# Optimization experiments

Measured on AMD Instinct MI355X. Metric: run time of the kernel, lower is better.

Reference implementation:

```python
import jax, jax.numpy as jnp
import numpy as np

N = 50000      # nodes
E = 800000     # edges (avg degree 16)
F_IN = 128     # num_features
HID = 128      # hidden_channels
C = 4          # num_labeled_classes


def setup_inputs() -> dict:
    key = jax.random.key(0)
    ks = jax.random.split(key, 12)
    x = jax.random.normal(ks[0], (N, F_IN), dtype=jnp.float32)
    edge_index = jax.random.randint(ks[1], (2, E), 0, N, dtype=jnp.int32)

    def lin(k, fan_in, fan_out):
        return (jax.random.normal(k, (fan_in, fan_out), dtype=jnp.float32)
                / np.float32(np.sqrt(fan_in)))

    return {
        "x": x,
        "edge_index": edge_index,
        # layer 0: SAGEConv(F_IN, HID) -> lin_l (with bias) on aggregated neighbors, lin_r on self
        "Wl0": lin(ks[2], F_IN, HID), "bl0": jnp.zeros((HID,), jnp.float32), "Wr0": lin(ks[3], F_IN, HID),
        # layer 1: SAGEConv(HID, HID)
        "Wl1": lin(ks[4], HID, HID), "bl1": jnp.zeros((HID,), jnp.float32), "Wr1": lin(ks[5], HID, HID),
        # layer 2: SAGEConv(HID, C)
        "Wl2": lin(ks[6], HID, C), "bl2": jnp.zeros((C,), jnp.float32), "Wr2": lin(ks[7], HID, C),
    }


def _sage_conv(x, src, dst, inv_deg, Wl, bl, Wr):
    # gather neighbor features [E, d], mean-aggregate at destination nodes
    msg = x[src]
    agg = jax.ops.segment_sum(msg, dst, num_segments=N)  # [N, d]
    mean = agg * inv_deg[:, None]
    # out = lin_l(mean_j) + lin_r(x_i)   (PyG SAGEConv default, mean aggr)
    return mean @ Wl + bl + x @ Wr


def reference(x, edge_index, Wl0, bl0, Wr0, Wl1, bl1, Wr1, Wl2, bl2, Wr2):
    src = edge_index[0]
    dst = edge_index[1]
    # in-degree of each destination node, clamped to 1 (isolated nodes -> 0 mean)
    deg = jax.ops.segment_sum(jnp.ones((E,), x.dtype), dst, num_segments=N)
    inv_deg = jnp.where(deg > 0, 1.0 / jnp.maximum(deg, 1.0), 0.0)

    h = _sage_conv(x, src, dst, inv_deg, Wl0, bl0, Wr0)
    h = jax.nn.relu(h)
    # dropout(p=0.5) is identity in eval mode
    h2 = _sage_conv(h, src, dst, inv_deg, Wl1, bl1, Wr1)
    out = _sage_conv(h2, src, dst, inv_deg, Wl2, bl2, Wr2)
    return (out, out, h2)
```

## Files before the change

### kernel.cpp

```cpp
#include <hip/hip_runtime.h>
#include <hip/hip_bf16.h>
#include <stdint.h>

#define NNODES 50000
#define NEDGES 800000
#define FDIM   128
#define NCLS   4
#define NB     196
#define ECAP   6144
#define LPITCH 136
#define NPH    8
#define SCAP   768

typedef uint32_t u32;
typedef unsigned char u8;
typedef unsigned short u16;
typedef __bf16 bf16x8 __attribute__((ext_vector_type(8)));
typedef float f32x4 __attribute__((ext_vector_type(4)));
typedef float f32x2 __attribute__((ext_vector_type(2)));

__device__ __forceinline__ u16 f2bf(float f) {
    u32 u = __float_as_uint(f);
    u32 r = u + 0x7fffu + ((u >> 16) & 1u);
    return (u16)(r >> 16);
}
__device__ __forceinline__ u32 pack2(float a, float b) {
    return (u32)f2bf(a) | ((u32)f2bf(b) << 16);
}
__device__ __forceinline__ float bflo(u32 p) { return __uint_as_float(p << 16); }
__device__ __forceinline__ float bfhi(u32 p) { return __uint_as_float(p & 0xffff0000u); }

__device__ __forceinline__ uint2 bf8x8_from_bf16(uint4 v) {
    uint2 o;
    o.x = __builtin_amdgcn_cvt_pk_fp8_f32(bflo(v.x), bfhi(v.x), 0,   false);
    o.x = __builtin_amdgcn_cvt_pk_fp8_f32(bflo(v.y), bfhi(v.y), o.x, true);
    o.y = __builtin_amdgcn_cvt_pk_fp8_f32(bflo(v.z), bfhi(v.z), 0,   false);
    o.y = __builtin_amdgcn_cvt_pk_fp8_f32(bflo(v.w), bfhi(v.w), o.y, true);
    return o;
}

__global__ void __launch_bounds__(256) k_pre(
        const int* __restrict__ dst,
        const float* __restrict__ Wl0, const float* __restrict__ Wr0,
        const float* __restrict__ Wl1, const float* __restrict__ Wr1,
        int* __restrict__ bcnt, u16* __restrict__ Bp0, u16* __restrict__ Bp1) {
    int t = threadIdx.x;
    int bid = blockIdx.x;
    if (bid < 782) {
        __shared__ int h[NB];
        if (t < NB) h[t] = 0;
        __syncthreads();
        int base = bid * 1024;
#pragma unroll
        for (int i = 0; i < 4; ++i) {
            int e = base + i * 256 + t;
            if (e < NEDGES) atomicAdd(&h[dst[e] >> 8], 1);
        }
        __syncthreads();
        if (t < NB) {
            int v = h[t];
            if (v) atomicAdd(&bcnt[t], v);
        }
    } else {
        int layer = (bid < 910) ? 0 : 1;
        int pid = bid - (layer ? 910 : 782);
        int tid = pid * 256 + t;
        int j    = tid & 7;
        int lane = (tid >> 3) & 63;
        int ks   = (tid >> 9) & 3;
        int nt   = tid >> 11;
        int col  = nt * 16 + (lane & 15);
        int k    = ks * 32 + (lane >> 4) * 8 + j;
        const float* Wl = layer ? Wl1 : Wl0;
        const float* Wr = layer ? Wr1 : Wr0;
        float v = (col < FDIM) ? Wl[k * FDIM + col] : Wr[k * FDIM + (col - FDIM)];
        (layer ? Bp1 : Bp0)[tid] = f2bf(v);
    }
}

__global__ void __launch_bounds__(256) k_scatmfma(
        const float* __restrict__ x, const uint4* __restrict__ Bp,
        const float* __restrict__ bias, u8* __restrict__ y, u16* __restrict__ zb,
        const int* __restrict__ src, const int* __restrict__ dst,
        const int* __restrict__ bcnt, int* __restrict__ bcur,
        u32* __restrict__ ebuf) {
    __shared__ u16 sA[64 * LPITCH];
    int t = threadIdx.x;
    if (blockIdx.x < 782) {
        int blk = blockIdx.x;
        int wave = t >> 6, lane = t & 63, m = lane & 15, quad = lane >> 4;
        {
            int row = t >> 2, q = t & 3;
            int r = blk * 64 + row;
            if (r >= NNODES) r = NNODES - 1;
            const float4* gs = (const float4*)(x + (size_t)r * FDIM) + q * 8;
            uint4* ld = (uint4*)(sA + row * LPITCH + q * 32);
#pragma unroll
            for (int i = 0; i < 4; ++i) {
                float4 a = gs[2 * i], b = gs[2 * i + 1];
                uint4 v;
                v.x = pack2(a.x, a.y); v.y = pack2(a.z, a.w);
                v.z = pack2(b.x, b.y); v.w = pack2(b.z, b.w);
                ld[i] = v;
            }
        }
        uint4 breg[4][4];
#pragma unroll
        for (int ks = 0; ks < 4; ++ks)
#pragma unroll
            for (int nt = 0; nt < 4; ++nt)
                breg[ks][nt] = Bp[((wave * 4 + nt) * 4 + ks) * 64 + lane];
        __syncthreads();
        bf16x8 a[4][4];
#pragma unroll
        for (int mt = 0; mt < 4; ++mt)
#pragma unroll
            for (int ks = 0; ks < 4; ++ks)
                a[mt][ks] = __builtin_bit_cast(bf16x8,
                    *(const uint4*)(sA + (mt * 16 + m) * LPITCH + ks * 32 + quad * 8));
        f32x4 acc[4][4];
#pragma unroll
        for (int mt = 0; mt < 4; ++mt)
#pragma unroll
            for (int nt = 0; nt < 4; ++nt) acc[mt][nt] = (f32x4){0.f, 0.f, 0.f, 0.f};
#pragma unroll
        for (int ks = 0; ks < 4; ++ks)
#pragma unroll
            for (int nt = 0; nt < 4; ++nt) {
                bf16x8 b = __builtin_bit_cast(bf16x8, breg[ks][nt]);
#pragma unroll
                for (int mt = 0; mt < 4; ++mt)
                    acc[mt][nt] = __builtin_amdgcn_mfma_f32_16x16x32_bf16(
                        a[mt][ks], b, acc[mt][nt], 0, 0, 0);
            }
        __syncthreads();
        if (wave < 2) {
#pragma unroll
            for (int nt = 0; nt < 4; ++nt) {
                int col = (wave * 4 + nt) * 16 + m;
#pragma unroll
                for (int mt = 0; mt < 4; ++mt)
#pragma unroll
                    for (int r = 0; r < 4; ++r)
                        sA[(mt * 16 + quad * 4 + r) * LPITCH + col] = f2bf(acc[mt][nt][r]);
            }
        }
        __syncthreads();
#pragma unroll
        for (int i = 0; i < 4; ++i) {
            int g = i * 256 + t, row = g >> 4, ch = g & 15;
            int gr = blk * 64 + row;
            if (gr < NNODES) {
                uint4 v = *(const uint4*)(sA + row * LPITCH + ch * 8);
                *((uint2*)(y + (size_t)gr * FDIM) + ch) = bf8x8_from_bf16(v);
            }
        }
        __syncthreads();
        if (wave >= 2) {
#pragma unroll
            for (int nt = 0; nt < 4; ++nt) {
                int col = (wave * 4 + nt) * 16 + m - 128;
                float bv = bias[col];
#pragma unroll
                for (int mt = 0; mt < 4; ++mt)
#pragma unroll
                    for (int r = 0; r < 4; ++r)
                        sA[(mt * 16 + quad * 4 + r) * LPITCH + col] = f2bf(acc[mt][nt][r] + bv);
            }
        }
        __syncthreads();
#pragma unroll
        for (int i = 0; i < 4; ++i) {
            int g = i * 256 + t, row = g >> 4, ch = g & 15;
            int gr = blk * 64 + row;
            if (gr < NNODES)
                *((uint4*)(zb + (size_t)gr * FDIM) + ch) =
                    *(const uint4*)(sA + row * LPITCH + ch * 8);
        }
    } else {
        int* hh = (int*)sA;
        int* bb = hh + 256;
        int* ss = bb + 256;
        int v = (t < NB) ? bcnt[t] : 0;
        ss[t] = v;
        __syncthreads();
        for (int off = 1; off < 256; off <<= 1) {
            int u = (t >= off) ? ss[t - off] : 0;
            __syncthreads();
            ss[t] += u;
            __syncthreads();
        }
        int boff = ss[t] - v;
        hh[t] = 0;
        __syncthreads();
        int eb = (blockIdx.x - 782) * 1024;
        int mb[4];
        u32 pk[4];
#pragma unroll
        for (int i = 0; i < 4; ++i) {
            int e = eb + i * 256 + t;
            if (e < NEDGES) {
                int d = dst[e];
                mb[i] = d >> 8;
                pk[i] = (u32)src[e] | ((u32)d << 16);
                atomicAdd(&hh[mb[i]], 1);
            } else mb[i] = -1;
        }
        __syncthreads();
        if (t < NB) {
            int c = hh[t];
            bb[t] = c ? (boff + atomicAdd(&bcur[t], c)) : 0;
            hh[t] = 0;
        }
        __syncthreads();
#pragma unroll
        for (int i = 0; i < 4; ++i) {
            if (mb[i] >= 0) {
                int r = atomicAdd(&hh[mb[i]], 1);
                ebuf[bb[mb[i]] + r] = pk[i];
            }
        }
    }
}

__global__ void __launch_bounds__(256) k_bfinal(
        const u32* __restrict__ ebuf, const int* __restrict__ bcnt,
        int* __restrict__ offs, float* __restrict__ invd, int* __restrict__ csr) {
    __shared__ u32 se[ECAP];
    __shared__ int deg8[256 * NPH];
    __shared__ int s[256];
    int b = blockIdx.x, t = threadIdx.x;
    int nbase = b << 8;
    int v = (t < NB) ? bcnt[t] : 0;
    s[t] = v;
    __syncthreads();
    for (int off = 1; off < 256; off <<= 1) {
        int u = (t >= off) ? s[t - off] : 0;
        __syncthreads();
        s[t] += u;
        __syncthreads();
    }
    int ebeg = s[b] - bcnt[b];
    int ecnt = bcnt[b];
    __syncthreads();
#pragma unroll
    for (int j = 0; j < NPH; ++j) deg8[t * NPH + j] = 0;
    __syncthreads();
    for (int i = t; i < ecnt; i += 256) {
        u32 e = ebuf[ebeg + i];
        if (i < ECAP) se[i] = e;
        atomicAdd(&deg8[((int)(e >> 16) - nbase) * NPH + (((int)(e & 0xffffu)) >> 13)], 1);
    }
    __syncthreads();
    int pre[NPH];
    int run = 0;
#pragma unroll
    for (int j = 0; j < NPH; ++j) { pre[j] = run; run += deg8[t * NPH + j]; }
    int d = run;
    s[t] = d;
    __syncthreads();
    for (int off = 1; off < 256; off <<= 1) {
        int u = (t >= off) ? s[t - off] : 0;
        __syncthreads();
        s[t] += u;
        __syncthreads();
    }
    int ex = s[t] - d;
    int node = nbase + t;
    if (node < NNODES) {
        offs[node] = ebeg + ex;
        invd[node] = (d > 0) ? (1.0f / (float)d) : 0.0f;
    }
    __syncthreads();
#pragma unroll
    for (int j = 0; j < NPH; ++j) deg8[t * NPH + j] = ex + pre[j];
    __syncthreads();
    for (int i = t; i < ecnt; i += 256) {
        u32 e = (i < ECAP) ? se[i] : ebuf[ebeg + i];
        int dl = (int)(e >> 16) - nbase;
        int sv = (int)(e & 0xffffu);
        int r = atomicAdd(&deg8[dl * NPH + (sv >> 13)], 1);
        csr[ebeg + r] = sv;
    }
    if (b == 0 && t == 0) offs[NNODES] = NEDGES;
}

template <int RELU, int OUTBF, int FUSE4>
__global__ void __launch_bounds__(256) k_agg(
        const u8* __restrict__ y, const int* __restrict__ offs,
        const int* __restrict__ csr, const float* __restrict__ invd,
        const u16* __restrict__ zb, u16* __restrict__ outb, float* __restrict__ outf,
        const float* __restrict__ Wl2, const float* __restrict__ Wr2,
        const float* __restrict__ bl2, float* __restrict__ y4,
        float* __restrict__ outz) {
    __shared__ int sidx[SCAP];
    int t = threadIdx.x;
    int n0 = blockIdx.x * 16;
    int base0 = offs[n0];
    int ecnt = offs[n0 + 16] - base0;
    for (int i = t; i < ecnt && i < SCAP; i += 256) sidx[i] = csr[base0 + i];
    __syncthreads();
    int nl = t >> 4, q = t & 15;
    int n = n0 + nl;
    int beg = offs[n], end = offs[n + 1];
    float a0 = 0, a1 = 0, a2 = 0, a3 = 0, a4 = 0, a5 = 0, a6 = 0, a7 = 0;
    const u8* yq = y + q * 8;
    int ii = beg;
    for (; ii + 4 <= end; ii += 4) {
        int li = ii - base0;
        int s0, s1, s2, s3;
        if (li + 3 < SCAP) {
            s0 = sidx[li]; s1 = sidx[li + 1]; s2 = sidx[li + 2]; s3 = sidx[li + 3];
        } else {
            s0 = csr[ii]; s1 = csr[ii + 1]; s2 = csr[ii + 2]; s3 = csr[ii + 3];
        }
        uint2 v0 = *(const uint2*)(yq + (size_t)s0 * FDIM);
        uint2 v1 = *(const uint2*)(yq + (size_t)s1 * FDIM);
        uint2 v2 = *(const uint2*)(yq + (size_t)s2 * FDIM);
        uint2 v3 = *(const uint2*)(yq + (size_t)s3 * FDIM);
#pragma unroll
        for (int j = 0; j < 4; ++j) {
            uint2 v = (j == 0) ? v0 : (j == 1) ? v1 : (j == 2) ? v2 : v3;
            f32x2 p0 = __builtin_amdgcn_cvt_pk_f32_fp8(v.x, false);
            f32x2 p1 = __builtin_amdgcn_cvt_pk_f32_fp8(v.x, true);
            f32x2 p2 = __builtin_amdgcn_cvt_pk_f32_fp8(v.y, false);
            f32x2 p3 = __builtin_amdgcn_cvt_pk_f32_fp8(v.y, true);
            a0 += p0.x; a1 += p0.y; a2 += p1.x; a3 += p1.y;
            a4 += p2.x; a5 += p2.y; a6 += p3.x; a7 += p3.y;
        }
    }
    for (; ii < end; ++ii) {
        int li = ii - base0;
        int s = (li < SCAP) ? sidx[li] : csr[ii];
        uint2 v = *(const uint2*)(yq + (size_t)s * FDIM);
        f32x2 p0 = __builtin_amdgcn_cvt_pk_f32_fp8(v.x, false);
        f32x2 p1 = __builtin_amdgcn_cvt_pk_f32_fp8(v.x, true);
        f32x2 p2 = __builtin_amdgcn_cvt_pk_f32_fp8(v.y, false);
        f32x2 p3 = __builtin_amdgcn_cvt_pk_f32_fp8(v.y, true);
        a0 += p0.x; a1 += p0.y; a2 += p1.x; a3 += p1.y;
        a4 += p2.x; a5 += p2.y; a6 += p3.x; a7 += p3.y;
    }
    float iv = invd[n];
    uint4 zv = *(const uint4*)(zb + (size_t)n * FDIM + q * 8);
    float r0 = fmaf(a0, iv, bflo(zv.x)), r1 = fmaf(a1, iv, bfhi(zv.x));
    float r2 = fmaf(a2, iv, bflo(zv.y)), r3 = fmaf(a3, iv, bfhi(zv.y));
    float r4 = fmaf(a4, iv, bflo(zv.z)), r5 = fmaf(a5, iv, bfhi(zv.z));
    float r6 = fmaf(a6, iv, bflo(zv.w)), r7 = fmaf(a7, iv, bfhi(zv.w));
    if (RELU) {
        r0 = fmaxf(r0, 0.f); r1 = fmaxf(r1, 0.f); r2 = fmaxf(r2, 0.f); r3 = fmaxf(r3, 0.f);
        r4 = fmaxf(r4, 0.f); r5 = fmaxf(r5, 0.f); r6 = fmaxf(r6, 0.f); r7 = fmaxf(r7, 0.f);
    }
    if (OUTBF) {
        uint4 o;
        o.x = pack2(r0, r1); o.y = pack2(r2, r3);
        o.z = pack2(r4, r5); o.w = pack2(r6, r7);
        *(uint4*)(outb + (size_t)n * FDIM + q * 8) = o;
    } else {
        float* o = outf + (size_t)n * FDIM + q * 8;
        ((float4*)o)[0] = make_float4(r0, r1, r2, r3);
        ((float4*)o)[1] = make_float4(r4, r5, r6, r7);
    }
    if (FUSE4) {
        float rr[8] = {r0, r1, r2, r3, r4, r5, r6, r7};
        float4 py = {0, 0, 0, 0}, pz = {0, 0, 0, 0};
        const float4* wl4 = (const float4*)Wl2;
        const float4* wr4 = (const float4*)Wr2;
#pragma unroll
        for (int j = 0; j < 8; ++j) {
            float4 wl = wl4[q * 8 + j], wr = wr4[q * 8 + j];
            py.x += rr[j] * wl.x; py.y += rr[j] * wl.y;
            py.z += rr[j] * wl.z; py.w += rr[j] * wl.w;
            pz.x += rr[j] * wr.x; pz.y += rr[j] * wr.y;
            pz.z += rr[j] * wr.z; pz.w += rr[j] * wr.w;
        }
#pragma unroll
        for (int off = 1; off < 16; off <<= 1) {
            py.x += __shfl_xor(py.x, off, 16); py.y += __shfl_xor(py.y, off, 16);
            py.z += __shfl_xor(py.z, off, 16); py.w += __shfl_xor(py.w, off, 16);
            pz.x += __shfl_xor(pz.x, off, 16); pz.y += __shfl_xor(pz.y, off, 16);
            pz.z += __shfl_xor(pz.z, off, 16); pz.w += __shfl_xor(pz.w, off, 16);
        }
        if (q == 0) {
            ((float4*)y4)[n] = py;
            float4 b2 = *(const float4*)bl2;
            float4 o;
            o.x = pz.x + b2.x; o.y = pz.y + b2.y;
            o.z = pz.z + b2.z; o.w = pz.w + b2.w;
            ((float4*)outz)[n] = o;
        }
    }
}

__global__ void __launch_bounds__(256) k_mfma1(
        const u16* __restrict__ in, const uint4* __restrict__ Bp,
        const float* __restrict__ bias, u8* __restrict__ y, u16* __restrict__ zb) {
    __shared__ u16 sA[64 * LPITCH];
    int t = threadIdx.x;
    int blk = blockIdx.x;
    int wave = t >> 6, lane = t & 63, m = lane & 15, quad = lane >> 4;
    {
        int row = t >> 2, q = t & 3;
        int r = blk * 64 + row;
        if (r >= NNODES) r = NNODES - 1;
        const uint4* gsrc = (const uint4*)(in + (size_t)r * FDIM);
        uint4* ldst = (uint4*)(sA + row * LPITCH);
#pragma unroll
        for (int i = 0; i < 4; ++i) ldst[q * 4 + i] = gsrc[q * 4 + i];
    }
    uint4 breg[4][4];
#pragma unroll
    for (int ks = 0; ks < 4; ++ks)
#pragma unroll
        for (int nt = 0; nt < 4; ++nt)
            breg[ks][nt] = Bp[((wave * 4 + nt) * 4 + ks) * 64 + lane];
    __syncthreads();
    bf16x8 a[4][4];
#pragma unroll
    for (int mt = 0; mt < 4; ++mt)
#pragma unroll
        for (int ks = 0; ks < 4; ++ks)
            a[mt][ks] = __builtin_bit_cast(bf16x8,
                *(const uint4*)(sA + (mt * 16 + m) * LPITCH + ks * 32 + quad * 8));
    f32x4 acc[4][4];
#pragma unroll
    for (int mt = 0; mt < 4; ++mt)
#pragma unroll
        for (int nt = 0; nt < 4; ++nt) acc[mt][nt] = (f32x4){0.f, 0.f, 0.f, 0.f};
#pragma unroll
    for (int ks = 0; ks < 4; ++ks)
#pragma unroll
        for (int nt = 0; nt < 4; ++nt) {
            bf16x8 b = __builtin_bit_cast(bf16x8, breg[ks][nt]);
#pragma unroll
            for (int mt = 0; mt < 4; ++mt)
                acc[mt][nt] = __builtin_amdgcn_mfma_f32_16x16x32_bf16(
                    a[mt][ks], b, acc[mt][nt], 0, 0, 0);
        }
    __syncthreads();
    if (wave < 2) {
#pragma unroll
        for (int nt = 0; nt < 4; ++nt) {
            int col = (wave * 4 + nt) * 16 + m;
#pragma unroll
            for (int mt = 0; mt < 4; ++mt)
#pragma unroll
                for (int r = 0; r < 4; ++r)
                    sA[(mt * 16 + quad * 4 + r) * LPITCH + col] = f2bf(acc[mt][nt][r]);
        }
    }
    __syncthreads();
#pragma unroll
    for (int i = 0; i < 4; ++i) {
        int g = i * 256 + t, row = g >> 4, ch = g & 15;
        int gr = blk * 64 + row;
        if (gr < NNODES) {
            uint4 v = *(const uint4*)(sA + row * LPITCH + ch * 8);
            *((uint2*)(y + (size_t)gr * FDIM) + ch) = bf8x8_from_bf16(v);
        }
    }
    __syncthreads();
    if (wave >= 2) {
#pragma unroll
        for (int nt = 0; nt < 4; ++nt) {
            int col = (wave * 4 + nt) * 16 + m - 128;
            float bv = bias[col];
#pragma unroll
            for (int mt = 0; mt < 4; ++mt)
#pragma unroll
                for (int r = 0; r < 4; ++r)
                    sA[(mt * 16 + quad * 4 + r) * LPITCH + col] = f2bf(acc[mt][nt][r] + bv);
        }
    }
    __syncthreads();
#pragma unroll
    for (int i = 0; i < 4; ++i) {
        int g = i * 256 + t, row = g >> 4, ch = g & 15;
        int gr = blk * 64 + row;
        if (gr < NNODES)
            *((uint4*)(zb + (size_t)gr * FDIM) + ch) =
                *(const uint4*)(sA + row * LPITCH + ch * 8);
    }
}

__global__ void k_agg4(const float* __restrict__ y4,
                       const int* __restrict__ offs,
                       const int* __restrict__ csr,
                       const float* __restrict__ invd,
                       float* __restrict__ out) {
    int tid = blockIdx.x * blockDim.x + threadIdx.x;
    int n = tid >> 2, c = tid & 3;
    if (n >= NNODES) return;
    int beg = offs[n], end = offs[n + 1];
    float acc = 0;
    int i = beg;
    for (; i + 4 <= end; i += 4) {
        int s0 = csr[i], s1 = csr[i + 1], s2 = csr[i + 2], s3 = csr[i + 3];
        float v0 = y4[(size_t)s0 * 4 + c];
        float v1 = y4[(size_t)s1 * 4 + c];
        float v2 = y4[(size_t)s2 * 4 + c];
        float v3 = y4[(size_t)s3 * 4 + c];
        acc += v0; acc += v1; acc += v2; acc += v3;
    }
    for (; i < end; ++i) acc += y4[(size_t)csr[i] * 4 + c];
    float r = fmaf(acc, invd[n], out[(size_t)n * 4 + c]);
    out[(size_t)n * 4 + c] = r;
    out[(size_t)NNODES * NCLS + (size_t)n * 4 + c] = r;
}

extern "C" void kernel_launch(void* const* d_in, const int* in_sizes, int n_in,
                              void* d_out, int out_size, void* d_ws, size_t ws_size,
                              hipStream_t stream) {
    const float* x   = (const float*)d_in[0];
    const int* ei    = (const int*)d_in[1];
    const float* Wl0 = (const float*)d_in[2];
    const float* bl0 = (const float*)d_in[3];
    const float* Wr0 = (const float*)d_in[4];
    const float* Wl1 = (const float*)d_in[5];
    const float* bl1 = (const float*)d_in[6];
    const float* Wr1 = (const float*)d_in[7];
    const float* Wl2 = (const float*)d_in[8];
    const float* bl2 = (const float*)d_in[9];
    const float* Wr2 = (const float*)d_in[10];

    const int* src = ei;
    const int* dst = ei + NEDGES;

    float* out = (float*)d_out;
    float* h2  = out + 2 * (size_t)NNODES * NCLS;

    char* ws = (char*)d_ws;
    int*   offs = (int*)(ws + 0);
    float* invd = (float*)(ws + 200192);
    int*   bcnt = (int*)(ws + 400384);
    int*   bcur = (int*)(ws + 401408);
    int*   csr  = (int*)(ws + 402432);
    u8*    y    = (u8*)(ws + 3602432);
    u16*   hb   = (u16*)(ws + 16402432);
    u16*   zb   = (u16*)(ws + 29202432);
    u32*   ebuf = (u32*)hb;
    float* y4   = (float*)(ws + 42002432);
    u16*   Bp0  = (u16*)(ws + 42802432);
    u16*   Bp1  = (u16*)(ws + 42867968);

    hipMemsetAsync(bcnt, 0, 2048, stream);

    k_pre<<<1038, 256, 0, stream>>>(dst, Wl0, Wr0, Wl1, Wr1, bcnt, Bp0, Bp1);

    k_scatmfma<<<1564, 256, 0, stream>>>(x, (const uint4*)Bp0, bl0, y, zb,
                                         src, dst, bcnt, bcur, ebuf);

    k_bfinal<<<NB, 256, 0, stream>>>(ebuf, bcnt, offs, invd, csr);

    k_agg<1, 1, 0><<<NNODES / 16, 256, 0, stream>>>(
        y, offs, csr, invd, zb, hb, nullptr,
        nullptr, nullptr, nullptr, nullptr, nullptr);

    k_mfma1<<<(NNODES + 63) / 64, 256, 0, stream>>>(hb, (const uint4*)Bp1, bl1, y, zb);

    k_agg<0, 0, 1><<<NNODES / 16, 256, 0, stream>>>(
        y, offs, csr, invd, zb, nullptr, h2,
        Wl2, Wr2, bl2, y4, out);

    k_agg4<<<(NNODES * NCLS + 255) / 256, 256, 0, stream>>>(y4, offs, csr, invd, out);
}
```

Baseline: 233.4 us.

## Fuse layer-0 aggregation with layer-1 MFMA projection into one kernel

Merges the first mean-aggregation kernel and the following bf16 MFMA projection kernel. Each 64-node block now gathers fp8 neighbor rows, applies ReLU, stages the hidden rows in LDS and multiplies them directly. This drops the intermediate hidden-state write and re-read plus one launch. Because the fused kernel reads y0 while writing y1, the two projections now use separate buffers, and ebuf gets its own region. The gather loops are also unrolled to 8 outstanding loads. The risk is fewer, heavier blocks with a serial 4-node-per-group gather and more register pressure.

```diff
diff --git a/kernel.cpp b/kernel.cpp
--- a/kernel.cpp
+++ b/kernel.cpp
@@ -11,6 +11,7 @@
 #define LPITCH 136
 #define NPH    8
 #define SCAP   768
+#define SCAP2  1536
 
 typedef uint32_t u32;
 typedef unsigned char u8;
@@ -37,6 +38,16 @@
     o.y = __builtin_amdgcn_cvt_pk_fp8_f32(bflo(v.z), bfhi(v.z), 0,   false);
     o.y = __builtin_amdgcn_cvt_pk_fp8_f32(bflo(v.w), bfhi(v.w), o.y, true);
     return o;
+}
+__device__ __forceinline__ void acc8(uint2 v, float& a0, float& a1, float& a2,
+                                     float& a3, float& a4, float& a5, float& a6,
+                                     float& a7) {
+    f32x2 p0 = __builtin_amdgcn_cvt_pk_f32_fp8(v.x, false);
+    f32x2 p1 = __builtin_amdgcn_cvt_pk_f32_fp8(v.x, true);
+    f32x2 p2 = __builtin_amdgcn_cvt_pk_f32_fp8(v.y, false);
+    f32x2 p3 = __builtin_amdgcn_cvt_pk_f32_fp8(v.y, true);
+    a0 += p0.x; a1 += p0.y; a2 += p1.x; a3 += p1.y;
+    a4 += p2.x; a5 += p2.y; a6 += p3.x; a7 += p3.y;
 }
 
 __global__ void __launch_bounds__(256) k_pre(
@@ -285,6 +296,145 @@
     if (b == 0 && t == 0) offs[NNODES] = NEDGES;
 }
 
+__global__ void __launch_bounds__(256) k_aggmfma(
+        const u8* __restrict__ y0, const int* __restrict__ offs,
+        const int* __restrict__ csr, const float* __restrict__ invd,
+        const uint4* __restrict__ Bp, const float* __restrict__ bias,
+        u8* __restrict__ y1, u16* __restrict__ zb) {
+    __shared__ u16 sA[64 * LPITCH];
+    __shared__ int sidx[SCAP2];
+    int t = threadIdx.x;
+    int blk = blockIdx.x;
+    int n0 = blk * 64;
+    int nend = (n0 + 64 < NNODES) ? (n0 + 64) : NNODES;
+    int base0 = offs[n0];
+    int ecnt = offs[nend] - base0;
+    for (int i = t; i < ecnt && i < SCAP2; i += 256) sidx[i] = csr[base0 + i];
+    __syncthreads();
+    int g = t >> 4, q = t & 15;
+    const u8* yq = y0 + q * 8;
+#pragma unroll
+    for (int j = 0; j < 4; ++j) {
+        int lr = g * 4 + j;
+        int n = n0 + lr;
+        uint4 hout = make_uint4(0, 0, 0, 0);
+        if (n < NNODES) {
+            int beg = offs[n], end = offs[n + 1];
+            float a0 = 0, a1 = 0, a2 = 0, a3 = 0, a4 = 0, a5 = 0, a6 = 0, a7 = 0;
+            int ii = beg;
+            for (; ii + 8 <= end; ii += 8) {
+                int li = ii - base0;
+                int s[8];
+                if (li + 7 < SCAP2) {
+#pragma unroll
+                    for (int k = 0; k < 8; ++k) s[k] = sidx[li + k];
+                } else {
+#pragma unroll
+                    for (int k = 0; k < 8; ++k) s[k] = csr[ii + k];
+                }
+                uint2 v[8];
+#pragma unroll
+                for (int k = 0; k < 8; ++k)
+                    v[k] = *(const uint2*)(yq + (size_t)s[k] * FDIM);
+#pragma unroll
+                for (int k = 0; k < 8; ++k)
+                    acc8(v[k], a0, a1, a2, a3, a4, a5, a6, a7);
+            }
+            for (; ii < end; ++ii) {
+                int li = ii - base0;
+                int s = (li < SCAP2) ? sidx[li] : csr[ii];
+                uint2 v = *(const uint2*)(yq + (size_t)s * FDIM);
+                acc8(v, a0, a1, a2, a3, a4, a5, a6, a7);
+            }
+            float iv = invd[n];
+            uint4 zv = *(const uint4*)(zb + (size_t)n * FDIM + q * 8);
+            float r0 = fmaxf(fmaf(a0, iv, bflo(zv.x)), 0.f);
+            float r1 = fmaxf(fmaf(a1, iv, bfhi(zv.x)), 0.f);
+            float r2 = fmaxf(fmaf(a2, iv, bflo(zv.y)), 0.f);
+            float r3 = fmaxf(fmaf(a3, iv, bfhi(zv.y)), 0.f);
+            float r4 = fmaxf(fmaf(a4, iv, bflo(zv.z)), 0.f);
+            float r5 = fmaxf(fmaf(a5, iv, bfhi(zv.z)), 0.f);
+            float r6 = fmaxf(fmaf(a6, iv, bflo(zv.w)), 0.f);
+            float r7 = fmaxf(fmaf(a7, iv, bfhi(zv.w)), 0.f);
+            hout.x = pack2(r0, r1); hout.y = pack2(r2, r3);
+            hout.z = pack2(r4, r5); hout.w = pack2(r6, r7);
+        }
+        *(uint4*)(sA + lr * LPITCH + q * 8) = hout;
+    }
+    __syncthreads();
+
+    int wave = t >> 6, lane = t & 63, m = lane & 15, quad = lane >> 4;
+    f32x4 acc[4][4];
+#pragma unroll
+    for (int mt = 0; mt < 4; ++mt)
+#pragma unroll
+        for (int nt = 0; nt < 4; ++nt) acc[mt][nt] = (f32x4){0.f, 0.f, 0.f, 0.f};
+#pragma unroll
+    for (int ks = 0; ks < 4; ++ks) {
+        uint4 breg[4];
+#pragma unroll
+        for (int nt = 0; nt < 4; ++nt)
+            breg[nt] = Bp[((wave * 4 + nt) * 4 + ks) * 64 + lane];
+        bf16x8 a[4];
+#pragma unroll
+        for (int mt = 0; mt < 4; ++mt)
+            a[mt] = __builtin_bit_cast(bf16x8,
+                *(const uint4*)(sA + (mt * 16 + m) * LPITCH + ks * 32 + quad * 8));
+#pragma unroll
+        for (int nt = 0; nt < 4; ++nt) {
+            bf16x8 b = __builtin_bit_cast(bf16x8, breg[nt]);
+#pragma unroll
+            for (int mt = 0; mt < 4; ++mt)
+                acc[mt][nt] = __builtin_amdgcn_mfma_f32_16x16x32_bf16(
+                    a[mt], b, acc[mt][nt], 0, 0, 0);
+        }
+    }
+    __syncthreads();
+    if (wave < 2) {
+#pragma unroll
+        for (int nt = 0; nt < 4; ++nt) {
+            int col = (wave * 4 + nt) * 16 + m;
+#pragma unroll
+            for (int mt = 0; mt < 4; ++mt)
+#pragma unroll
+                for (int r = 0; r < 4; ++r)
+                    sA[(mt * 16 + quad * 4 + r) * LPITCH + col] = f2bf(acc[mt][nt][r]);
+        }
+    }
+    __syncthreads();
+#pragma unroll
+    for (int i = 0; i < 4; ++i) {
+        int gg = i * 256 + t, row = gg >> 4, ch = gg & 15;
+        int gr = n0 + row;
+        if (gr < NNODES) {
+            uint4 v = *(const uint4*)(sA + row * LPITCH + ch * 8);
+            *((uint2*)(y1 + (size_t)gr * FDIM) + ch) = bf8x8_from_bf16(v);
+        }
+    }
+    __syncthreads();
+    if (wave >= 2) {
+#pragma unroll
+        for (int nt = 0; nt < 4; ++nt) {
+            int col = (wave * 4 + nt) * 16 + m - 128;
+            float bv = bias[col];
+#pragma unroll
+            for (int mt = 0; mt < 4; ++mt)
+#pragma unroll
+                for (int r = 0; r < 4; ++r)
+                    sA[(mt * 16 + quad * 4 + r) * LPITCH + col] = f2bf(acc[mt][nt][r] + bv);
+        }
+    }
+    __syncthreads();
+#pragma unroll
+    for (int i = 0; i < 4; ++i) {
+        int gg = i * 256 + t, row = gg >> 4, ch = gg & 15;
+        int gr = n0 + row;
+        if (gr < NNODES)
+            *((uint4*)(zb + (size_t)gr * FDIM) + ch) =
+                *(const uint4*)(sA + row * LPITCH + ch * 8);
+    }
+}
+
 template <int RELU, int OUTBF, int FUSE4>
 __global__ void __launch_bounds__(256) k_agg(
         const u8* __restrict__ y, const int* __restrict__ offs,
@@ -306,39 +456,29 @@
     float a0 = 0, a1 = 0, a2 = 0, a3 = 0, a4 = 0, a5 = 0, a6 = 0, a7 = 0;
     const u8* yq = y + q * 8;
     int ii = beg;
-    for (; ii + 4 <= end; ii += 4) {
+    for (; ii + 8 <= end; ii += 8) {
         int li = ii - base0;
-        int s0, s1, s2, s3;
-        if (li + 3 < SCAP) {
-            s0 = sidx[li]; s1 = sidx[li + 1]; s2 = sidx[li + 2]; s3 = sidx[li + 3];
+        int s[8];
+        if (li + 7 < SCAP) {
+#pragma unroll
+            for (int k = 0; k < 8; ++k) s[k] = sidx[li + k];
         } else {
-            s0 = csr[ii]; s1 = csr[ii + 1]; s2 = csr[ii + 2]; s3 = csr[ii + 3];
-        }
-        uint2 v0 = *(const uint2*)(yq + (size_t)s0 * FDIM);
-        uint2 v1 = *(const uint2*)(yq + (size_t)s1 * FDIM);
-        uint2 v2 = *(const uint2*)(yq + (size_t)s2 * FDIM);
-        uint2 v3 = *(const uint2*)(yq + (size_t)s3 * FDIM);
-#pragma unroll
-        for (int j = 0; j < 4; ++j) {
-            uint2 v = (j == 0) ? v0 : (j == 1) ? v1 : (j == 2) ? v2 : v3;
-            f32x2 p0 = __builtin_amdgcn_cvt_pk_f32_fp8(v.x, false);
-            f32x2 p1 = __builtin_amdgcn_cvt_pk_f32_fp8(v.x, true);
-            f32x2 p2 = __builtin_amdgcn_cvt_pk_f32_fp8(v.y, false);
-            f32x2 p3 = __builtin_amdgcn_cvt_pk_f32_fp8(v.y, true);
-            a0 += p0.x; a1 += p0.y; a2 += p1.x; a3 += p1.y;
-            a4 += p2.x; a5 += p2.y; a6 += p3.x; a7 += p3.y;
-        }
+#pragma unroll
+            for (int k = 0; k < 8; ++k) s[k] = csr[ii + k];
+        }
+        uint2 v[8];
+#pragma unroll
+        for (int k = 0; k < 8; ++k)
+            v[k] = *(const uint2*)(yq + (size_t)s[k] * FDIM);
+#pragma unroll
+        for (int k = 0; k < 8; ++k)
+            acc8(v[k], a0, a1, a2, a3, a4, a5, a6, a7);
     }
     for (; ii < end; ++ii) {
         int li = ii - base0;
         int s = (li < SCAP) ? sidx[li] : csr[ii];
         uint2 v = *(const uint2*)(yq + (size_t)s * FDIM);
-        f32x2 p0 = __builtin_amdgcn_cvt_pk_f32_fp8(v.x, false);
-        f32x2 p1 = __builtin_amdgcn_cvt_pk_f32_fp8(v.x, true);
-        f32x2 p2 = __builtin_amdgcn_cvt_pk_f32_fp8(v.y, false);
-        f32x2 p3 = __builtin_amdgcn_cvt_pk_f32_fp8(v.y, true);
-        a0 += p0.x; a1 += p0.y; a2 += p1.x; a3 += p1.y;
-        a4 += p2.x; a5 += p2.y; a6 += p3.x; a7 += p3.y;
+        acc8(v, a0, a1, a2, a3, a4, a5, a6, a7);
     }
     float iv = invd[n];
     uint4 zv = *(const uint4*)(zb + (size_t)n * FDIM + q * 8);
@@ -388,97 +528,6 @@
             o.z = pz.z + b2.z; o.w = pz.w + b2.w;
             ((float4*)outz)[n] = o;
         }
-    }
-}
-
-__global__ void __launch_bounds__(256) k_mfma1(
-        const u16* __restrict__ in, const uint4* __restrict__ Bp,
-        const float* __restrict__ bias, u8* __restrict__ y, u16* __restrict__ zb) {
-    __shared__ u16 sA[64 * LPITCH];
-    int t = threadIdx.x;
-    int blk = blockIdx.x;
-    int wave = t >> 6, lane = t & 63, m = lane & 15, quad = lane >> 4;
-    {
-        int row = t >> 2, q = t & 3;
-        int r = blk * 64 + row;
-        if (r >= NNODES) r = NNODES - 1;
-        const uint4* gsrc = (const uint4*)(in + (size_t)r * FDIM);
-        uint4* ldst = (uint4*)(sA + row * LPITCH);
-#pragma unroll
-        for (int i = 0; i < 4; ++i) ldst[q * 4 + i] = gsrc[q * 4 + i];
-    }
-    uint4 breg[4][4];
-#pragma unroll
-    for (int ks = 0; ks < 4; ++ks)
-#pragma unroll
-        for (int nt = 0; nt < 4; ++nt)
-            breg[ks][nt] = Bp[((wave * 4 + nt) * 4 + ks) * 64 + lane];
-    __syncthreads();
-    bf16x8 a[4][4];
-#pragma unroll
-    for (int mt = 0; mt < 4; ++mt)
-#pragma unroll
-        for (int ks = 0; ks < 4; ++ks)
-            a[mt][ks] = __builtin_bit_cast(bf16x8,
-                *(const uint4*)(sA + (mt * 16 + m) * LPITCH + ks * 32 + quad * 8));
-    f32x4 acc[4][4];
-#pragma unroll
-    for (int mt = 0; mt < 4; ++mt)
-#pragma unroll
-        for (int nt = 0; nt < 4; ++nt) acc[mt][nt] = (f32x4){0.f, 0.f, 0.f, 0.f};
-#pragma unroll
-    for (int ks = 0; ks < 4; ++ks)
-#pragma unroll
-        for (int nt = 0; nt < 4; ++nt) {
-            bf16x8 b = __builtin_bit_cast(bf16x8, breg[ks][nt]);
-#pragma unroll
-            for (int mt = 0; mt < 4; ++mt)
-                acc[mt][nt] = __builtin_amdgcn_mfma_f32_16x16x32_bf16(
-                    a[mt][ks], b, acc[mt][nt], 0, 0, 0);
-        }
-    __syncthreads();
-    if (wave < 2) {
-#pragma unroll
-        for (int nt = 0; nt < 4; ++nt) {
-            int col = (wave * 4 + nt) * 16 + m;
-#pragma unroll
-            for (int mt = 0; mt < 4; ++mt)
-#pragma unroll
-                for (int r = 0; r < 4; ++r)
-                    sA[(mt * 16 + quad * 4 + r) * LPITCH + col] = f2bf(acc[mt][nt][r]);
-        }
-    }
-    __syncthreads();
-#pragma unroll
-    for (int i = 0; i < 4; ++i) {
-        int g = i * 256 + t, row = g >> 4, ch = g & 15;
-        int gr = blk * 64 + row;
-        if (gr < NNODES) {
-            uint4 v = *(const uint4*)(sA + row * LPITCH + ch * 8);
-            *((uint2*)(y + (size_t)gr * FDIM) + ch) = bf8x8_from_bf16(v);
-        }
-    }
-    __syncthreads();
-    if (wave >= 2) {
-#pragma unroll
-        for (int nt = 0; nt < 4; ++nt) {
-            int col = (wave * 4 + nt) * 16 + m - 128;
-            float bv = bias[col];
-#pragma unroll
-            for (int mt = 0; mt < 4; ++mt)
-#pragma unroll
-                for (int r = 0; r < 4; ++r)
-                    sA[(mt * 16 + quad * 4 + r) * LPITCH + col] = f2bf(acc[mt][nt][r] + bv);
-        }
-    }
-    __syncthreads();
-#pragma unroll
-    for (int i = 0; i < 4; ++i) {
-        int g = i * 256 + t, row = g >> 4, ch = g & 15;
-        int gr = blk * 64 + row;
-        if (gr < NNODES)
-            *((uint4*)(zb + (size_t)gr * FDIM) + ch) =
-                *(const uint4*)(sA + row * LPITCH + ch * 8);
     }
 }
 
@@ -534,10 +583,10 @@
     int*   bcnt = (int*)(ws + 400384);
     int*   bcur = (int*)(ws + 401408);
     int*   csr  = (int*)(ws + 402432);
-    u8*    y    = (u8*)(ws + 3602432);
-    u16*   hb   = (u16*)(ws + 16402432);
+    u8*    y0   = (u8*)(ws + 3602432);
+    u8*    y1   = (u8*)(ws + 16402432);
+    u32*   ebuf = (u32*)(ws + 22802432);
     u16*   zb   = (u16*)(ws + 29202432);
-    u32*   ebuf = (u32*)hb;
     float* y4   = (float*)(ws + 42002432);
     u16*   Bp0  = (u16*)(ws + 42802432);
     u16*   Bp1  = (u16*)(ws + 42867968);
@@ -546,19 +595,16 @@
 
     k_pre<<<1038, 256, 0, stream>>>(dst, Wl0, Wr0, Wl1, Wr1, bcnt, Bp0, Bp1);
 
-    k_scatmfma<<<1564, 256, 0, stream>>>(x, (const uint4*)Bp0, bl0, y, zb,
+    k_scatmfma<<<1564, 256, 0, stream>>>(x, (const uint4*)Bp0, bl0, y0, zb,
                                          src, dst, bcnt, bcur, ebuf);
 
     k_bfinal<<<NB, 256, 0, stream>>>(ebuf, bcnt, offs, invd, csr);
 
-    k_agg<1, 1, 0><<<NNODES / 16, 256, 0, stream>>>(
-        y, offs, csr, invd, zb, hb, nullptr,
-        nullptr, nullptr, nullptr, nullptr, nullptr);
-
-    k_mfma1<<<(NNODES + 63) / 64, 256, 0, stream>>>(hb, (const uint4*)Bp1, bl1, y, zb);
+    k_aggmfma<<<(NNODES + 63) / 64, 256, 0, stream>>>(
+        y0, offs, csr, invd, (const uint4*)Bp1, bl1, y1, zb);
 
     k_agg<0, 0, 1><<<NNODES / 16, 256, 0, stream>>>(
-        y, offs, csr, invd, zb, nullptr, h2,
+        y1, offs, csr, invd, zb, nullptr, h2,
         Wl2, Wr2, bl2, y4, out);
 
     k_agg4<<<(NNODES * NCLS + 255) / 256, 256, 0, stream>>>(y4, offs, csr, invd, out);
```

After: 248.5 us. +6.5%, slower.
